# Kernel optimization log

Hardware: AMD Instinct MI355X
Metric: run time of the kernel (lower is better)

Reference implementation:

```python
import jax, jax.numpy as jnp
import numpy as np

TEMPERATURE = 0.1
EPS = 1e-8  # torch cosine_similarity eps
NEG_FILL = -9e15

def setup_inputs() -> dict:
    key = jax.random.key(0)
    stacked_batch = jax.random.normal(key, (8192, 128), dtype=jnp.float32)
    return {"stacked_batch": stacked_batch}

def reference(stacked_batch) -> jnp.ndarray:
    n = stacked_batch.shape[0]
    # cosine similarity = normalized GEMM (equivalent to torch broadcast form)
    norm = jnp.maximum(jnp.linalg.norm(stacked_batch, axis=-1, keepdims=True), EPS)
    z = stacked_batch / norm                      # [N, D]
    sim = jnp.matmul(z, z.T) / TEMPERATURE        # [N, N]
    # mask self-similarity on the diagonal
    idx = jnp.arange(n)
    sim = sim.at[idx, idx].set(NEG_FILL)
    # positive pair for row i is column (i + N/2) mod N
    pos_cols = (idx + n // 2) % n
    pos = sim[idx, pos_cols]                      # [N]
    loss = jax.scipy.special.logsumexp(sim, axis=-1) - pos
    return loss.mean()
```

## Files before the change

### kernel.cpp

```cpp
#include <hip/hip_runtime.h>
#include <hip/hip_bf16.h>

#define N 8192
#define D 128
#define HALF_N 4096
#define SCALE 10.0f

#define BLOCK_ROWS 256
#define COLS_PER_ITER 64
#define COL_SPLITS 16
#define COLS_PER_BLOCK (N / COL_SPLITS)
#define ITERS (COLS_PER_BLOCK / COLS_PER_ITER)
#define LDS_STRIDE 136

typedef short frag8 __attribute__((ext_vector_type(8)));
typedef float f32x4 __attribute__((ext_vector_type(4)));

__device__ __forceinline__ unsigned short f2bf(float f) {
    unsigned int u = __float_as_uint(f);
    u += 0x7FFFu + ((u >> 16) & 1u);
    return (unsigned short)(u >> 16);
}

__global__ __launch_bounds__(64) void k_normalize(const float* __restrict__ x,
                                                  unsigned short* __restrict__ z,
                                                  float* __restrict__ sumexp,
                                                  float* __restrict__ pos) {
    const int row = blockIdx.x;
    const int lane = threadIdx.x;
    float2 v = ((const float2*)x)[row * 64 + lane];
    float s = v.x * v.x + v.y * v.y;
    #pragma unroll
    for (int m = 32; m >= 1; m >>= 1) s += __shfl_xor(s, m);
    float norm = fmaxf(sqrtf(s), 1e-8f);
    float inv = 1.0f / norm;
    ushort2 o;
    o.x = f2bf(v.x * inv);
    o.y = f2bf(v.y * inv);
    ((ushort2*)z)[row * 64 + lane] = o;
    if (lane == 0) sumexp[row] = 0.0f;
    if (lane == 1) pos[row] = 0.0f;
}

__global__ __launch_bounds__(256, 2) void k_simloss(const unsigned short* __restrict__ z,
                                                    float* __restrict__ sumexp,
                                                    float* __restrict__ pos) {
    __shared__ unsigned short lds[COLS_PER_ITER * LDS_STRIDE];

    const int tid  = threadIdx.x;
    const int wave = tid >> 6;
    const int lane = tid & 63;
    const int l15  = lane & 15;
    const int quad = lane >> 4;
    const int wrow = blockIdx.x * BLOCK_ROWS + wave * 64;
    const int colbase0 = blockIdx.y * COLS_PER_BLOCK;

    frag8 a[4][4];
    #pragma unroll
    for (int s = 0; s < 4; ++s) {
        const uint4* p = (const uint4*)&z[(wrow + s * 16 + l15) * D + quad * 8];
        #pragma unroll
        for (int q = 0; q < 4; ++q) {
            uint4 t = p[q * 4];
            a[s][q] = *(frag8*)&t;
        }
    }

    float sums[4][4];
    #pragma unroll
    for (int s = 0; s < 4; ++s)
        #pragma unroll
        for (int r = 0; r < 4; ++r) sums[s][r] = 0.0f;

    for (int it = 0; it < ITERS; ++it) {
        const int colbase = colbase0 + it * COLS_PER_ITER;
        __syncthreads();
        #pragma unroll
        for (int u = 0; u < 4; ++u) {
            int idx = u * 256 + tid;
            int r   = idx >> 4;
            int c8  = idx & 15;
            uint4 t = *(const uint4*)&z[(colbase + r) * D + c8 * 8];
            *(uint4*)&lds[r * LDS_STRIDE + c8 * 8] = t;
        }
        __syncthreads();

        const unsigned short* lp = &lds[l15 * LDS_STRIDE + quad * 8];
        #pragma unroll
        for (int c = 0; c < 4; ++c) {
            f32x4 acc[4];
            #pragma unroll
            for (int s = 0; s < 4; ++s) acc[s] = (f32x4){0.f, 0.f, 0.f, 0.f};
            #pragma unroll
            for (int q = 0; q < 4; ++q) {
                frag8 b = *(const frag8*)(lp + c * 16 * LDS_STRIDE + q * 32);
                #pragma unroll
                for (int s = 0; s < 4; ++s)
                    acc[s] = __builtin_amdgcn_mfma_f32_16x16x32_bf16(a[s][q], b, acc[s], 0, 0, 0);
            }
            const int gcol = colbase + c * 16 + l15;
            #pragma unroll
            for (int s = 0; s < 4; ++s) {
                const int growb = wrow + s * 16 + quad * 4;
                #pragma unroll
                for (int r = 0; r < 4; ++r) {
                    const int grow = growb + r;
                    float val = acc[s][r] * SCALE;
                    float e = __expf(val);
                    if (gcol == grow) e = 0.0f;
                    sums[s][r] += e;
                    if (gcol == ((grow + HALF_N) & (N - 1))) pos[grow] = val;
                }
            }
        }
    }

    #pragma unroll
    for (int s = 0; s < 4; ++s) {
        #pragma unroll
        for (int r = 0; r < 4; ++r) {
            float v = sums[s][r];
            v += __shfl_xor(v, 1);
            v += __shfl_xor(v, 2);
            v += __shfl_xor(v, 4);
            v += __shfl_xor(v, 8);
            if (l15 == 0) atomicAdd(&sumexp[wrow + s * 16 + quad * 4 + r], v);
        }
    }
}

__global__ __launch_bounds__(256) void k_finalize(const float* __restrict__ sumexp,
                                                  const float* __restrict__ pos,
                                                  float* __restrict__ out) {
    const int tid = threadIdx.x;
    float acc = 0.0f;
    for (int i = tid; i < N; i += 256)
        acc += logf(sumexp[i]) - pos[i];
    #pragma unroll
    for (int m = 32; m >= 1; m >>= 1) acc += __shfl_xor(acc, m);
    __shared__ float partial[4];
    if ((tid & 63) == 0) partial[tid >> 6] = acc;
    __syncthreads();
    if (tid == 0)
        out[0] = (partial[0] + partial[1] + partial[2] + partial[3]) * (1.0f / N);
}

extern "C" void kernel_launch(void* const* d_in, const int* in_sizes, int n_in,
                              void* d_out, int out_size, void* d_ws, size_t ws_size,
                              hipStream_t stream) {
    const float* x = (const float*)d_in[0];
    float* sumexp = (float*)d_ws;
    float* pos    = sumexp + N;
    unsigned short* z = (unsigned short*)((char*)d_ws + 2 * N * 4);

    k_normalize<<<N, 64, 0, stream>>>(x, z, sumexp, pos);
    dim3 g2(N / BLOCK_ROWS, COL_SPLITS);
    k_simloss<<<g2, 256, 0, stream>>>(z, sumexp, pos);
    k_finalize<<<1, 256, 0, stream>>>(sumexp, pos, (float*)d_out);
}
```

Before: 95.38 us.

## Fold scale into normalization, skip mask checks off-diagonal, deterministic partial sums

Folds the 1/temperature scale into the normalized bf16 vectors (multiplying each by sqrt(10)), so the epilogue drops the per-element multiply. Diagonal and positive-pair checks now run only on the 64-column tiles that can contain them, leaving the common path as a plain exp-and-add. The column split doubles with a higher occupancy hint for more blocks in flight. Per-block partial row sums go to a buffer instead of atomics, then a parallel row-loss kernel and a tiny final kernel reduce them. This costs an extra launch and a larger workspace, and the positive value now carries bf16 rounding of the pre-scaled vectors.

```diff
diff --git a/kernel.cpp b/kernel.cpp
--- a/kernel.cpp
+++ b/kernel.cpp
@@ -4,17 +4,22 @@
 #define N 8192
 #define D 128
 #define HALF_N 4096
-#define SCALE 10.0f
+#define SQRT_SCALE 3.16227766016838f
 
 #define BLOCK_ROWS 256
 #define COLS_PER_ITER 64
-#define COL_SPLITS 16
+#define COL_SPLITS 32
 #define COLS_PER_BLOCK (N / COL_SPLITS)
 #define ITERS (COLS_PER_BLOCK / COLS_PER_ITER)
 #define LDS_STRIDE 136
 
 typedef short frag8 __attribute__((ext_vector_type(8)));
 typedef float f32x4 __attribute__((ext_vector_type(4)));
+
+#define OFF_POS    0
+#define OFF_PSUMS  (N)
+#define OFF_ACC    (N + COL_SPLITS * N)
+#define OFF_Z_BYTES ((OFF_ACC + 64) * 4)
 
 __device__ __forceinline__ unsigned short f2bf(float f) {
     unsigned int u = __float_as_uint(f);
@@ -24,26 +29,23 @@
 
 __global__ __launch_bounds__(64) void k_normalize(const float* __restrict__ x,
                                                   unsigned short* __restrict__ z,
-                                                  float* __restrict__ sumexp,
-                                                  float* __restrict__ pos) {
+                                                  float* __restrict__ acc0) {
     const int row = blockIdx.x;
     const int lane = threadIdx.x;
     float2 v = ((const float2*)x)[row * 64 + lane];
     float s = v.x * v.x + v.y * v.y;
     #pragma unroll
     for (int m = 32; m >= 1; m >>= 1) s += __shfl_xor(s, m);
-    float norm = fmaxf(sqrtf(s), 1e-8f);
-    float inv = 1.0f / norm;
+    float inv = SQRT_SCALE / fmaxf(sqrtf(s), 1e-8f);
     ushort2 o;
     o.x = f2bf(v.x * inv);
     o.y = f2bf(v.y * inv);
     ((ushort2*)z)[row * 64 + lane] = o;
-    if (lane == 0) sumexp[row] = 0.0f;
-    if (lane == 1) pos[row] = 0.0f;
+    if (row == 0 && lane == 0) acc0[0] = 0.0f;
 }
 
-__global__ __launch_bounds__(256, 2) void k_simloss(const unsigned short* __restrict__ z,
-                                                    float* __restrict__ sumexp,
+__global__ __launch_bounds__(256, 4) void k_simloss(const unsigned short* __restrict__ z,
+                                                    float* __restrict__ psums,
                                                     float* __restrict__ pos) {
     __shared__ unsigned short lds[COLS_PER_ITER * LDS_STRIDE];
 
@@ -54,6 +56,7 @@
     const int quad = lane >> 4;
     const int wrow = blockIdx.x * BLOCK_ROWS + wave * 64;
     const int colbase0 = blockIdx.y * COLS_PER_BLOCK;
+    const int posbase  = (wrow + HALF_N) & (N - 1);
 
     frag8 a[4][4];
     #pragma unroll
@@ -85,7 +88,10 @@
         }
         __syncthreads();
 
+        const bool isDiag = (colbase == wrow);
+        const bool isPos  = (colbase == posbase);
         const unsigned short* lp = &lds[l15 * LDS_STRIDE + quad * 8];
+
         #pragma unroll
         for (int c = 0; c < 4; ++c) {
             f32x4 acc[4];
@@ -98,25 +104,32 @@
                 for (int s = 0; s < 4; ++s)
                     acc[s] = __builtin_amdgcn_mfma_f32_16x16x32_bf16(a[s][q], b, acc[s], 0, 0, 0);
             }
-            const int gcol = colbase + c * 16 + l15;
-            #pragma unroll
-            for (int s = 0; s < 4; ++s) {
-                const int growb = wrow + s * 16 + quad * 4;
+            if (isDiag | isPos) {
                 #pragma unroll
-                for (int r = 0; r < 4; ++r) {
-                    const int grow = growb + r;
-                    float val = acc[s][r] * SCALE;
-                    float e = __expf(val);
-                    if (gcol == grow) e = 0.0f;
-                    sums[s][r] += e;
-                    if (gcol == ((grow + HALF_N) & (N - 1))) pos[grow] = val;
-                }
+                for (int s = 0; s < 4; ++s)
+                    #pragma unroll
+                    for (int r = 0; r < 4; ++r) {
+                        float v = acc[s][r];
+                        float e = __expf(v);
+                        if (c == s) {
+                            bool hit = (l15 == quad * 4 + r);
+                            if (isDiag && hit) e = 0.0f;
+                            if (isPos  && hit) pos[wrow + s * 16 + quad * 4 + r] = v;
+                        }
+                        sums[s][r] += e;
+                    }
+            } else {
+                #pragma unroll
+                for (int s = 0; s < 4; ++s)
+                    #pragma unroll
+                    for (int r = 0; r < 4; ++r)
+                        sums[s][r] += __expf(acc[s][r]);
             }
         }
     }
 
     #pragma unroll
-    for (int s = 0; s < 4; ++s) {
+    for (int s = 0; s < 4; ++s)
         #pragma unroll
         for (int r = 0; r < 4; ++r) {
             float v = sums[s][r];
@@ -124,37 +137,49 @@
             v += __shfl_xor(v, 2);
             v += __shfl_xor(v, 4);
             v += __shfl_xor(v, 8);
-            if (l15 == 0) atomicAdd(&sumexp[wrow + s * 16 + quad * 4 + r], v);
+            if (l15 == 0)
+                psums[blockIdx.y * N + wrow + s * 16 + quad * 4 + r] = v;
         }
+}
+
+__global__ __launch_bounds__(1024) void k_rowloss(const float* __restrict__ psums,
+                                                  const float* __restrict__ pos,
+                                                  float* __restrict__ acc0) {
+    const int row = blockIdx.x * 1024 + threadIdx.x;
+    float t = 0.0f;
+    #pragma unroll
+    for (int s = 0; s < COL_SPLITS; ++s) t += psums[s * N + row];
+    float loss = __logf(t) - pos[row];
+    #pragma unroll
+    for (int m = 32; m >= 1; m >>= 1) loss += __shfl_xor(loss, m);
+    __shared__ float p[16];
+    if ((threadIdx.x & 63) == 0) p[threadIdx.x >> 6] = loss;
+    __syncthreads();
+    if (threadIdx.x == 0) {
+        float s = 0.0f;
+        #pragma unroll
+        for (int w = 0; w < 16; ++w) s += p[w];
+        atomicAdd(acc0, s);
     }
 }
 
-__global__ __launch_bounds__(256) void k_finalize(const float* __restrict__ sumexp,
-                                                  const float* __restrict__ pos,
-                                                  float* __restrict__ out) {
-    const int tid = threadIdx.x;
-    float acc = 0.0f;
-    for (int i = tid; i < N; i += 256)
-        acc += logf(sumexp[i]) - pos[i];
-    #pragma unroll
-    for (int m = 32; m >= 1; m >>= 1) acc += __shfl_xor(acc, m);
-    __shared__ float partial[4];
-    if ((tid & 63) == 0) partial[tid >> 6] = acc;
-    __syncthreads();
-    if (tid == 0)
-        out[0] = (partial[0] + partial[1] + partial[2] + partial[3]) * (1.0f / N);
+__global__ void k_final(const float* __restrict__ acc0, float* __restrict__ out) {
+    out[0] = acc0[0] * (1.0f / N);
 }
 
 extern "C" void kernel_launch(void* const* d_in, const int* in_sizes, int n_in,
                               void* d_out, int out_size, void* d_ws, size_t ws_size,
                               hipStream_t stream) {
     const float* x = (const float*)d_in[0];
-    float* sumexp = (float*)d_ws;
-    float* pos    = sumexp + N;
-    unsigned short* z = (unsigned short*)((char*)d_ws + 2 * N * 4);
+    float* wsf   = (float*)d_ws;
+    float* pos   = wsf + OFF_POS;
+    float* psums = wsf + OFF_PSUMS;
+    float* acc0  = wsf + OFF_ACC;
+    unsigned short* z = (unsigned short*)((char*)d_ws + OFF_Z_BYTES);
 
-    k_normalize<<<N, 64, 0, stream>>>(x, z, sumexp, pos);
+    k_normalize<<<N, 64, 0, stream>>>(x, z, acc0);
     dim3 g2(N / BLOCK_ROWS, COL_SPLITS);
-    k_simloss<<<g2, 256, 0, stream>>>(z, sumexp, pos);
-    k_finalize<<<1, 256, 0, stream>>>(sumexp, pos, (float*)d_out);
+    k_simloss<<<g2, 256, 0, stream>>>(z, psums, pos);
+    k_rowloss<<<N / 1024, 1024, 0, stream>>>(psums, pos, acc0);
+    k_final<<<1, 1, 0, stream>>>(acc0, (float*)d_out);
 }
```

Measured after the change: 174.4 us. 1.83x slower.
